# Kernel optimization log

Measured on AMD Instinct MI355X. Metric: run time of the kernel, lower is better.

The kernel has to match this reference:

```python
import jax, jax.numpy as jnp
import numpy as np

B, S, D_IN, H, G, HD = 1, 2048, 2048, 32, 8, 128
GS = H // G  # group_size = 4
D_OUT = H * HD  # 4096
EPS = 1e-6


def _rmsnorm(x, scale):
    # qwen3-compatible: compute in fp32 over last dim
    xf = x.astype(jnp.float32)
    var = jnp.mean(xf * xf, axis=-1, keepdims=True)
    return (xf * jax.lax.rsqrt(var + EPS) * scale).astype(x.dtype)


def _apply_rope(x, cos, sin):
    # x: [b, h, s, d]; cos/sin: [s, d]
    d2 = x.shape[-1] // 2
    x1, x2 = x[..., :d2], x[..., d2:]
    rotated = jnp.concatenate([-x2, x1], axis=-1)
    return (x * cos[None, None] + rotated * sin[None, None]).astype(x.dtype)


def setup_inputs() -> dict:
    key = jax.random.key(0)
    ks = jax.random.split(key, 8)
    x = jax.random.normal(ks[0], (B, S, D_IN), jnp.float32)
    mask = jnp.triu(jnp.ones((S, S), bool), k=1)  # causal: True = masked
    # RoPE tables [S, HD]
    inv_freq = 1.0 / (10000.0 ** (jnp.arange(0, HD, 2, dtype=jnp.float32) / HD))
    ang = jnp.arange(S, dtype=jnp.float32)[:, None] * inv_freq[None, :]
    ang = jnp.concatenate([ang, ang], axis=-1)
    cos, sin = jnp.cos(ang), jnp.sin(ang)
    std = 0.02
    Wq = jax.random.normal(ks[1], (D_IN, D_OUT), jnp.float32) * std
    Wk = jax.random.normal(ks[2], (D_IN, G * HD), jnp.float32) * std
    Wv = jax.random.normal(ks[3], (D_IN, G * HD), jnp.float32) * std
    Wo = jax.random.normal(ks[4], (D_OUT, D_IN), jnp.float32) * std
    q_scale = jnp.ones((HD,), jnp.float32)
    k_scale = jnp.ones((HD,), jnp.float32)
    return {"x": x, "mask": mask, "cos": cos, "sin": sin,
            "Wq": Wq, "Wk": Wk, "Wv": Wv, "Wo": Wo,
            "q_scale": q_scale, "k_scale": k_scale}


def reference(x, mask, cos, sin, Wq, Wk, Wv, Wo, q_scale, k_scale):
    b, s, _ = x.shape
    q = (x @ Wq).reshape(b, s, H, HD).transpose(0, 2, 1, 3)   # [b,H,s,hd]
    k = (x @ Wk).reshape(b, s, G, HD).transpose(0, 2, 1, 3)   # [b,G,s,hd]
    v = (x @ Wv).reshape(b, s, G, HD).transpose(0, 2, 1, 3)   # [b,G,s,hd]
    q = _rmsnorm(q, q_scale)
    k = _rmsnorm(k, k_scale)
    q = _apply_rope(q, cos[:s], sin[:s])
    k = _apply_rope(k, cos[:s], sin[:s])
    next_k, next_v = k, v  # cache (num_kv_groups heads)
    # GQA via broadcasting instead of repeat_interleave (same math)
    qg = q.reshape(b, G, GS, s, HD)
    scores = jnp.einsum('bgrsd,bgtd->bgrst', qg, k)           # [b,G,gs,s,s]
    scores = jnp.where(mask[None, None, None], -jnp.inf, scores)
    attn = jax.nn.softmax(scores / np.sqrt(HD).astype(np.float32), axis=-1)
    ctx = jnp.einsum('bgrst,bgtd->bgrsd', attn, v)            # [b,G,gs,s,hd]
    ctx = ctx.reshape(b, H, s, HD).transpose(0, 2, 1, 3).reshape(b, s, D_OUT)
    out = ctx @ Wo
    return out, next_k, next_v
```

## Files before the change

kernel.cpp:

```cpp
#include <hip/hip_runtime.h>

typedef unsigned short ushort_t;
typedef short short8 __attribute__((ext_vector_type(8)));
typedef float floatx4 __attribute__((ext_vector_type(4)));

#define S_LEN 2048
#define DIN   2048
#define NH    32
#define NG    8
#define HDIM  128
#define DOUT  4096
#define DKV   1024
#define QLD   6144

__device__ __forceinline__ float b2f(ushort_t u) {
  union { float f; unsigned u; } t; t.u = ((unsigned)u) << 16; return t.f;
}
__device__ __forceinline__ ushort_t f2b(float f) {
  union { float f; unsigned u; } t; t.f = f;
  unsigned v = t.u;
  v += 0x7FFFu + ((v >> 16) & 1u);
  return (ushort_t)(v >> 16);
}

__device__ __forceinline__ void glds16(const ushort_t* g, ushort_t* l) {
  __builtin_amdgcn_global_load_lds((const __attribute__((address_space(1))) void*)g,
                                   (__attribute__((address_space(3))) void*)l, 16, 0, 0);
}

__global__ __launch_bounds__(256) void tcast(const float* __restrict__ W,
                                             ushort_t* __restrict__ Wt,
                                             int N, int ldt) {
  __shared__ float t[32][33];
  const int bx = blockIdx.x * 32;
  const int by = blockIdx.y * 32;
  const int tx = threadIdx.x & 31;
  const int ty = threadIdx.x >> 5;
#pragma unroll
  for (int i = 0; i < 32; i += 8)
    t[ty + i][tx] = W[(size_t)(by + ty + i) * N + bx + tx];
  __syncthreads();
#pragma unroll
  for (int i = 0; i < 32; i += 8)
    Wt[(size_t)(bx + ty + i) * ldt + by + tx] = f2b(t[tx][ty + i]);
}

__global__ __launch_bounds__(256) void castx(const float* __restrict__ x,
                                             ushort_t* __restrict__ xb) {
  const size_t i = ((size_t)blockIdx.x * 256 + threadIdx.x) * 4;
  float4 v = *(const float4*)&x[i];
  union { int2 p; ushort_t s[4]; } w;
  w.s[0] = f2b(v.x); w.s[1] = f2b(v.y); w.s[2] = f2b(v.z); w.s[3] = f2b(v.w);
  *(int2*)&xb[i] = w.p;
}

template <int CF32, int BM>
__global__ __launch_bounds__(256) void gemm_glds(const ushort_t* __restrict__ A, int lda,
                                                 const ushort_t* __restrict__ Bt, int ldb,
                                                 void* __restrict__ Cp, int ldc, int K) {
  constexpr int MI = BM / 32;
  __shared__ __align__(16) ushort_t As[BM * 32];
  __shared__ __align__(16) ushort_t Bs[4096];
  const int tid  = threadIdx.x;
  const int m0   = blockIdx.y * BM;
  const int n0   = blockIdx.x * 128;
  const int wave = tid >> 6, lane = tid & 63;
  const int lrow = lane & 15, quad = lane >> 4;
  const int wm = (wave >> 1) * (BM / 2), wn = (wave & 1) * 64;

  floatx4 acc[MI][4];
#pragma unroll
  for (int mi = 0; mi < MI; mi++)
#pragma unroll
    for (int ni = 0; ni < 4; ni++)
#pragma unroll
      for (int j = 0; j < 4; j++) acc[mi][ni][j] = 0.0f;

  const ushort_t* ag0 = A + (size_t)(m0 + (tid >> 2)) * lda + (tid & 3) * 8;
  const ushort_t* ag1 = ag0 + (size_t)64 * lda;
  const ushort_t* bg0 = Bt + (size_t)(n0 + (tid >> 2)) * ldb + (tid & 3) * 8;
  const ushort_t* bg1 = bg0 + (size_t)64 * ldb;
  ushort_t* lA0 = As + wave * 512;
  ushort_t* lA1 = As + 2048 + wave * 512;
  ushort_t* lB0 = Bs + wave * 512;
  ushort_t* lB1 = Bs + 2048 + wave * 512;

  for (int k0 = 0; k0 < K; k0 += 32) {
    __syncthreads();
    glds16(ag0 + k0, lA0);
    if (BM == 128) glds16(ag1 + k0, lA1);
    glds16(bg0 + k0, lB0);
    glds16(bg1 + k0, lB1);
    __syncthreads();

    short8 af[MI], bf[4];
#pragma unroll
    for (int mi = 0; mi < MI; mi++)
      af[mi] = *(const short8*)&As[(wm + mi * 16 + lrow) * 32 + quad * 8];
#pragma unroll
    for (int ni = 0; ni < 4; ni++)
      bf[ni] = *(const short8*)&Bs[(wn + ni * 16 + lrow) * 32 + quad * 8];
#pragma unroll
    for (int mi = 0; mi < MI; mi++)
#pragma unroll
      for (int ni = 0; ni < 4; ni++)
        acc[mi][ni] = __builtin_amdgcn_mfma_f32_16x16x32_bf16(af[mi], bf[ni], acc[mi][ni], 0, 0, 0);
  }

#pragma unroll
  for (int mi = 0; mi < MI; mi++)
#pragma unroll
    for (int ni = 0; ni < 4; ni++)
#pragma unroll
      for (int i = 0; i < 4; i++) {
        const int row = m0 + wm + mi * 16 + quad * 4 + i;
        const int col = n0 + wn + ni * 16 + lrow;
        if (CF32) ((float*)Cp)[(size_t)row * ldc + col] = acc[mi][ni][i];
        else      ((ushort_t*)Cp)[(size_t)row * ldc + col] = f2b(acc[mi][ni][i]);
      }
}

__global__ __launch_bounds__(256) void norm_qk(ushort_t* __restrict__ qkv,
                                               const float* __restrict__ cosb,
                                               const float* __restrict__ sinb,
                                               const float* __restrict__ qs,
                                               const float* __restrict__ ks,
                                               ushort_t* __restrict__ kb) {
  const int idx  = blockIdx.x * 4 + (threadIdx.x >> 6);
  const int lane = threadIdx.x & 63;
  const int SH = S_LEN * NH;
  const float QSC = 0.08838834764831845f * 1.4426950408889634f;

  if (idx < SH) {
    const int s = idx >> 5, h = idx & 31;
    ushort_t* row = qkv + (size_t)s * QLD + h * HDIM;
    float x1 = b2f(row[lane]), x2 = b2f(row[lane + 64]);
    float ss = x1 * x1 + x2 * x2;
#pragma unroll
    for (int off = 1; off < 64; off <<= 1) ss += __shfl_xor(ss, off);
    const float inv = rsqrtf(ss * (1.0f / 128.0f) + 1e-6f);
    const float y1 = x1 * inv * qs[lane] * QSC;
    const float y2 = x2 * inv * qs[lane + 64] * QSC;
    const float c1 = cosb[s * HDIM + lane],      s1 = sinb[s * HDIM + lane];
    const float c2 = cosb[s * HDIM + lane + 64], s2 = sinb[s * HDIM + lane + 64];
    row[lane]      = f2b(y1 * c1 - y2 * s1);
    row[lane + 64] = f2b(y2 * c2 + y1 * s2);
  } else {
    const int j = idx - SH;
    const int s = j >> 3, g = j & 7;
    const ushort_t* row = qkv + (size_t)s * QLD + DOUT + g * HDIM;
    float x1 = b2f(row[lane]), x2 = b2f(row[lane + 64]);
    float ss = x1 * x1 + x2 * x2;
#pragma unroll
    for (int off = 1; off < 64; off <<= 1) ss += __shfl_xor(ss, off);
    const float inv = rsqrtf(ss * (1.0f / 128.0f) + 1e-6f);
    const float y1 = x1 * inv * ks[lane];
    const float y2 = x2 * inv * ks[lane + 64];
    const float c1 = cosb[s * HDIM + lane],      s1 = sinb[s * HDIM + lane];
    const float c2 = cosb[s * HDIM + lane + 64], s2 = sinb[s * HDIM + lane + 64];
    ushort_t* o = kb + ((size_t)g * S_LEN + s) * HDIM;
    o[lane]      = f2b(y1 * c1 - y2 * s1);
    o[lane + 64] = f2b(y2 * c2 + y1 * s2);
  }
}

__global__ __launch_bounds__(256) void vtrans(const ushort_t* __restrict__ qkv,
                                              ushort_t* __restrict__ vt) {
  __shared__ ushort_t t[64][65];
  const int g = blockIdx.x;
  const int s0 = blockIdx.y * 64, d0 = blockIdx.z * 64;
  const int tx = threadIdx.x & 63, ty = threadIdx.x >> 6;
#pragma unroll
  for (int i = 0; i < 64; i += 4)
    t[ty + i][tx] = qkv[(size_t)(s0 + ty + i) * QLD + DOUT + DKV + g * HDIM + d0 + tx];
  __syncthreads();
#pragma unroll
  for (int i = 0; i < 64; i += 4)
    vt[((size_t)(g * HDIM + d0 + ty + i)) * S_LEN + s0 + tx] = t[tx][ty + i];
}

__global__ __launch_bounds__(256, 2) void attn(ushort_t* QC,
                                               const ushort_t* __restrict__ Kb,
                                               const ushort_t* __restrict__ Vt) {
  __shared__ __align__(16) ushort_t Ks[8192];
  __shared__ __align__(16) ushort_t Vs[8192];
  __shared__ __align__(16) ushort_t Ps[64 * 72];
  const int h  = blockIdx.x;
  const int qt = 31 - blockIdx.y;
  const int g  = h >> 2;
  const int tid = threadIdx.x;
  const int wave = tid >> 6, lane = tid & 63;
  const int lrow = lane & 15, quad = lane >> 4;
  const ushort_t* Kg = Kb + (size_t)g * S_LEN * HDIM;
  const ushort_t* Vg = Vt + (size_t)g * HDIM * S_LEN;
  const int r0 = qt * 64;
  const int qrow0 = r0 + wave * 16;

  short8 qf[4];
#pragma unroll
  for (int kd = 0; kd < 4; kd++)
    qf[kd] = *(const short8*)&QC[(size_t)(qrow0 + lrow) * QLD + h * HDIM + kd * 32 + quad * 8];

  short8 vones;
#pragma unroll
  for (int j = 0; j < 8; j++) vones[j] = (lrow == 0) ? (short)0x3F80 : (short)0;

  floatx4 ctx[8], ctxl;
#pragma unroll
  for (int nd = 0; nd < 8; nd++)
#pragma unroll
    for (int j = 0; j < 4; j++) ctx[nd][j] = 0.0f;
#pragma unroll
  for (int j = 0; j < 4; j++) ctxl[j] = 0.0f;

  const ushort_t* kgl = Kg + (size_t)(wave * 16 + (lane >> 2)) * HDIM + (lane & 3) * 8;
  const ushort_t* vgl = Vg + (size_t)(wave * 32 + (lane >> 2)) * S_LEN + (lane & 3) * 8;

  for (int t0 = 0; t0 <= r0; t0 += 64) {
    __syncthreads();
#pragma unroll
    for (int i = 0; i < 4; i++)
      glds16(kgl + (size_t)t0 * HDIM + i * 32, Ks + i * 2048 + wave * 512);
#pragma unroll
    for (int i = 0; i < 4; i++)
      glds16(vgl + (size_t)((i >> 1) * 16) * S_LEN + t0 + (i & 1) * 32,
             Vs + (i & 1) * 4096 + (wave * 32 + (i >> 1) * 16) * 32);
    __syncthreads();

    floatx4 sacc[4];
#pragma unroll
    for (int ni = 0; ni < 4; ni++)
#pragma unroll
      for (int j = 0; j < 4; j++) sacc[ni][j] = 0.0f;
#pragma unroll
    for (int kd = 0; kd < 4; kd++) {
      short8 kf[4];
#pragma unroll
      for (int ni = 0; ni < 4; ni++)
        kf[ni] = *(const short8*)&Ks[kd * 2048 + (ni * 16 + lrow) * 32 + quad * 8];
#pragma unroll
      for (int ni = 0; ni < 4; ni++)
        sacc[ni] = __builtin_amdgcn_mfma_f32_16x16x32_bf16(qf[kd], kf[ni], sacc[ni], 0, 0, 0);
    }

    const bool diag = (t0 == r0);
#pragma unroll
    for (int ni = 0; ni < 4; ni++)
#pragma unroll
      for (int i = 0; i < 4; i++) {
        float sv = sacc[ni][i];
        if (diag && (t0 + ni * 16 + lrow > qrow0 + quad * 4 + i)) sv = -1e30f;
        sacc[ni][i] = exp2f(sv - 17.0f);
      }

#pragma unroll
    for (int ni = 0; ni < 4; ni++)
#pragma unroll
      for (int i = 0; i < 4; i++)
        Ps[(wave * 16 + quad * 4 + i) * 72 + ni * 16 + lrow] = f2b(sacc[ni][i]);
    asm volatile("s_waitcnt lgkmcnt(0)" ::: "memory");

#pragma unroll
    for (int kt = 0; kt < 2; kt++) {
      const short8 pf = *(const short8*)&Ps[(wave * 16 + lrow) * 72 + kt * 32 + quad * 8];
      ctxl = __builtin_amdgcn_mfma_f32_16x16x32_bf16(pf, vones, ctxl, 0, 0, 0);
#pragma unroll
      for (int nd = 0; nd < 8; nd++) {
        const short8 vf = *(const short8*)&Vs[kt * 4096 + (nd * 16 + lrow) * 32 + quad * 8];
        ctx[nd] = __builtin_amdgcn_mfma_f32_16x16x32_bf16(pf, vf, ctx[nd], 0, 0, 0);
      }
    }
  }

  float invl[4];
#pragma unroll
  for (int i = 0; i < 4; i++) invl[i] = 1.0f / __shfl(ctxl[i], lane & 48);

  __syncthreads();
  ushort_t* Es = (wave < 2) ? Ks : Vs;
  const int eb = (wave & 1) * 16;
#pragma unroll
  for (int i = 0; i < 4; i++)
#pragma unroll
    for (int nd = 0; nd < 8; nd++)
      Es[(eb + quad * 4 + i) * 136 + nd * 16 + lrow] = f2b(ctx[nd][i] * invl[i]);
  asm volatile("s_waitcnt lgkmcnt(0)" ::: "memory");
  const int erow = lane >> 4;
  const int ecol = (lane & 15) * 8;
#pragma unroll
  for (int rr = 0; rr < 4; rr++) {
    int4 v = *(const int4*)&Es[(eb + rr * 4 + erow) * 136 + ecol];
    *(int4*)&QC[(size_t)(r0 + wave * 16 + rr * 4 + erow) * QLD + h * HDIM + ecol] = v;
  }
}

__global__ __launch_bounds__(256) void fink(const ushort_t* __restrict__ kb,
                                            float* __restrict__ nk) {
  const size_t e = ((size_t)blockIdx.x * 256 + threadIdx.x) * 8;
  union { int4 v; ushort_t s[8]; } u;
  u.v = *(const int4*)&kb[e];
#pragma unroll
  for (int j = 0; j < 8; j++) nk[e + j] = b2f(u.s[j]);
}

__global__ __launch_bounds__(256) void finv(const ushort_t* __restrict__ qkv,
                                            float* __restrict__ nv) {
  const int s = blockIdx.x;
  const int g = threadIdx.x >> 5, d4 = (threadIdx.x & 31) * 4;
  union { short4 v; ushort_t s[4]; } u;
  u.v = *(const short4*)&qkv[(size_t)s * QLD + DOUT + DKV + g * HDIM + d4];
  float4 o;
  o.x = b2f(u.s[0]); o.y = b2f(u.s[1]); o.z = b2f(u.s[2]); o.w = b2f(u.s[3]);
  *(float4*)&nv[((size_t)g * S_LEN + s) * HDIM + d4] = o;
}

extern "C" void kernel_launch(void* const* d_in, const int* in_sizes, int n_in,
                              void* d_out, int out_size, void* d_ws, size_t ws_size,
                              hipStream_t stream) {
  const float* x    = (const float*)d_in[0];
  const float* cosb = (const float*)d_in[2];
  const float* sinb = (const float*)d_in[3];
  const float* Wq   = (const float*)d_in[4];
  const float* Wk   = (const float*)d_in[5];
  const float* Wv   = (const float*)d_in[6];
  const float* Wo   = (const float*)d_in[7];
  const float* qs   = (const float*)d_in[8];
  const float* ks   = (const float*)d_in[9];

  float* outf = (float*)d_out;
  float* nkf  = outf + (size_t)S_LEN * DIN;
  float* nvf  = nkf + (size_t)NG * S_LEN * HDIM;

  const size_t MiB = 1024 * 1024;
  ushort_t* WallT = (ushort_t*)d_out;
  ushort_t* xb    = (ushort_t*)((char*)d_out + 24 * MiB);
  ushort_t* WoT   = (ushort_t*)((char*)d_out + 16 * MiB);
  ushort_t* vt    = (ushort_t*)d_out;
  ushort_t* qkv   = (ushort_t*)d_ws;
  ushort_t* kb    = (ushort_t*)((char*)d_ws + 24 * MiB);

  tcast<<<dim3(128, 64), 256, 0, stream>>>(Wq, WallT, DOUT, DIN);
  tcast<<<dim3(32, 64), 256, 0, stream>>>(Wk, WallT + (size_t)4096 * DIN, DKV, DIN);
  tcast<<<dim3(32, 64), 256, 0, stream>>>(Wv, WallT + (size_t)5120 * DIN, DKV, DIN);
  castx<<<4096, 256, 0, stream>>>(x, xb);

  gemm_glds<0, 128><<<dim3(48, 16), 256, 0, stream>>>(xb, DIN, WallT, DIN, qkv, QLD, DIN);

  tcast<<<dim3(64, 128), 256, 0, stream>>>(Wo, WoT, DIN, DOUT);

  norm_qk<<<(S_LEN * NH + S_LEN * NG) / 4, 256, 0, stream>>>(qkv, cosb, sinb, qs, ks, kb);

  vtrans<<<dim3(NG, S_LEN / 64, HDIM / 64), 256, 0, stream>>>(qkv, vt);

  attn<<<dim3(NH, 32), 256, 0, stream>>>(qkv, kb, vt);

  gemm_glds<1, 64><<<dim3(16, 32), 256, 0, stream>>>(qkv, QLD, WoT, DOUT, outf, DIN, DOUT);

  fink<<<1024, 256, 0, stream>>>(kb, nkf);
  finv<<<S_LEN, 256, 0, stream>>>(qkv, nvf);
}
```

Baseline: 399.8 us.

## Double-buffer LDS tiles with XOR swizzle in GEMM and attention

Both the projection GEMM and the attention kernel now use two LDS buffers. The next K-tile (or K/V tile) is loaded directly into LDS while the current one is computed, which replaces the two-barrier load-then-compute loop with one barrier per step. The 16-byte column chunks are also XOR-swizzled on both the write and read side to cut LDS bank conflicts. The cost is double the shared memory: attention goes from about 41 KB to about 74 KB per block, which may reduce occupancy under launch_bounds(256,2). The GEMM loop also assumes K/32 is even, which holds for the K values used here.

```diff
diff --git a/kernel.cpp b/kernel.cpp
--- a/kernel.cpp
+++ b/kernel.cpp
@@ -59,8 +59,8 @@
                                                  const ushort_t* __restrict__ Bt, int ldb,
                                                  void* __restrict__ Cp, int ldc, int K) {
   constexpr int MI = BM / 32;
-  __shared__ __align__(16) ushort_t As[BM * 32];
-  __shared__ __align__(16) ushort_t Bs[4096];
+  __shared__ __align__(16) ushort_t As[2][BM * 32];
+  __shared__ __align__(16) ushort_t Bs[2][4096];
   const int tid  = threadIdx.x;
   const int m0   = blockIdx.y * BM;
   const int n0   = blockIdx.x * 128;
@@ -76,35 +76,51 @@
 #pragma unroll
       for (int j = 0; j < 4; j++) acc[mi][ni][j] = 0.0f;
 
-  const ushort_t* ag0 = A + (size_t)(m0 + (tid >> 2)) * lda + (tid & 3) * 8;
+  const int sc = ((tid & 3) ^ ((tid >> 3) & 3)) * 8;
+  const ushort_t* ag0 = A + (size_t)(m0 + (tid >> 2)) * lda + sc;
   const ushort_t* ag1 = ag0 + (size_t)64 * lda;
-  const ushort_t* bg0 = Bt + (size_t)(n0 + (tid >> 2)) * ldb + (tid & 3) * 8;
+  const ushort_t* bg0 = Bt + (size_t)(n0 + (tid >> 2)) * ldb + sc;
   const ushort_t* bg1 = bg0 + (size_t)64 * ldb;
-  ushort_t* lA0 = As + wave * 512;
-  ushort_t* lA1 = As + 2048 + wave * 512;
-  ushort_t* lB0 = Bs + wave * 512;
-  ushort_t* lB1 = Bs + 2048 + wave * 512;
-
-  for (int k0 = 0; k0 < K; k0 += 32) {
-    __syncthreads();
-    glds16(ag0 + k0, lA0);
-    if (BM == 128) glds16(ag1 + k0, lA1);
-    glds16(bg0 + k0, lB0);
-    glds16(bg1 + k0, lB1);
-    __syncthreads();
-
-    short8 af[MI], bf[4];
+  const int so = wave * 512;
+
+  auto stage = [&](int k0, int b) {
+    glds16(ag0 + k0, &As[b][so]);
+    if constexpr (BM == 128) glds16(ag1 + k0, &As[b][2048 + so]);
+    glds16(bg0 + k0, &Bs[b][so]);
+    glds16(bg1 + k0, &Bs[b][2048 + so]);
+  };
+
+  const int rq = (quad ^ ((lrow >> 1) & 3)) * 8;
+
+  auto compute = [&](int b) {
+    short8 af[MI], bfr[4];
 #pragma unroll
     for (int mi = 0; mi < MI; mi++)
-      af[mi] = *(const short8*)&As[(wm + mi * 16 + lrow) * 32 + quad * 8];
-#pragma unroll
-    for (int ni = 0; ni < 4; ni++)
-      bf[ni] = *(const short8*)&Bs[(wn + ni * 16 + lrow) * 32 + quad * 8];
+      af[mi] = *(const short8*)&As[b][(wm + mi * 16 + lrow) * 32 + rq];
+#pragma unroll
+    for (int ni = 0; ni < 4; ni++)
+      bfr[ni] = *(const short8*)&Bs[b][(wn + ni * 16 + lrow) * 32 + rq];
 #pragma unroll
     for (int mi = 0; mi < MI; mi++)
 #pragma unroll
       for (int ni = 0; ni < 4; ni++)
-        acc[mi][ni] = __builtin_amdgcn_mfma_f32_16x16x32_bf16(af[mi], bf[ni], acc[mi][ni], 0, 0, 0);
+        acc[mi][ni] = __builtin_amdgcn_mfma_f32_16x16x32_bf16(af[mi], bfr[ni], acc[mi][ni], 0, 0, 0);
+  };
+
+  stage(0, 0);
+  asm volatile("s_waitcnt vmcnt(0)" ::: "memory");
+  __builtin_amdgcn_s_barrier();
+
+  const int NT = K >> 5;
+  for (int t = 0; t < NT; t += 2) {
+    stage((t + 1) << 5, 1);
+    compute(0);
+    asm volatile("s_waitcnt vmcnt(0)" ::: "memory");
+    __builtin_amdgcn_s_barrier();
+    if (t + 2 < NT) stage((t + 2) << 5, 0);
+    compute(1);
+    asm volatile("s_waitcnt vmcnt(0)" ::: "memory");
+    __builtin_amdgcn_s_barrier();
   }
 
 #pragma unroll
@@ -182,8 +198,8 @@
 __global__ __launch_bounds__(256, 2) void attn(ushort_t* QC,
                                                const ushort_t* __restrict__ Kb,
                                                const ushort_t* __restrict__ Vt) {
-  __shared__ __align__(16) ushort_t Ks[8192];
-  __shared__ __align__(16) ushort_t Vs[8192];
+  __shared__ __align__(16) ushort_t Ks[2][8192];
+  __shared__ __align__(16) ushort_t Vs[2][8192];
   __shared__ __align__(16) ushort_t Ps[64 * 72];
   const int h  = blockIdx.x;
   const int qt = 31 - blockIdx.y;
@@ -213,19 +229,31 @@
 #pragma unroll
   for (int j = 0; j < 4; j++) ctxl[j] = 0.0f;
 
-  const ushort_t* kgl = Kg + (size_t)(wave * 16 + (lane >> 2)) * HDIM + (lane & 3) * 8;
-  const ushort_t* vgl = Vg + (size_t)(wave * 32 + (lane >> 2)) * S_LEN + (lane & 3) * 8;
-
-  for (int t0 = 0; t0 <= r0; t0 += 64) {
-    __syncthreads();
+  const int swz = ((lane & 3) ^ ((lane >> 3) & 3)) * 8;
+  const ushort_t* kgl = Kg + (size_t)(wave * 16 + (lane >> 2)) * HDIM + swz;
+  const ushort_t* vgl = Vg + (size_t)(wave * 32 + (lane >> 2)) * S_LEN + swz;
+
+  auto stageKV = [&](int t0, int b) {
 #pragma unroll
     for (int i = 0; i < 4; i++)
-      glds16(kgl + (size_t)t0 * HDIM + i * 32, Ks + i * 2048 + wave * 512);
+      glds16(kgl + (size_t)t0 * HDIM + i * 32, &Ks[b][i * 2048 + wave * 512]);
 #pragma unroll
     for (int i = 0; i < 4; i++)
       glds16(vgl + (size_t)((i >> 1) * 16) * S_LEN + t0 + (i & 1) * 32,
-             Vs + (i & 1) * 4096 + (wave * 32 + (i >> 1) * 16) * 32);
-    __syncthreads();
+             &Vs[b][(i & 1) * 4096 + (wave * 32 + (i >> 1) * 16) * 32]);
+  };
+
+  const int rq = (quad ^ ((lrow >> 1) & 3)) * 8;
+
+  stageKV(0, 0);
+  asm volatile("s_waitcnt vmcnt(0)" ::: "memory");
+  __builtin_amdgcn_s_barrier();
+
+  int buf = 0;
+  for (int t0 = 0; t0 <= r0; t0 += 64) {
+    if (t0 + 64 <= r0) stageKV(t0 + 64, buf ^ 1);
+    const ushort_t* Kc = Ks[buf];
+    const ushort_t* Vc = Vs[buf];
 
     floatx4 sacc[4];
 #pragma unroll
@@ -237,7 +265,7 @@
       short8 kf[4];
 #pragma unroll
       for (int ni = 0; ni < 4; ni++)
-        kf[ni] = *(const short8*)&Ks[kd * 2048 + (ni * 16 + lrow) * 32 + quad * 8];
+        kf[ni] = *(const short8*)&Kc[kd * 2048 + (ni * 16 + lrow) * 32 + rq];
 #pragma unroll
       for (int ni = 0; ni < 4; ni++)
         sacc[ni] = __builtin_amdgcn_mfma_f32_16x16x32_bf16(qf[kd], kf[ni], sacc[ni], 0, 0, 0);
@@ -266,10 +294,14 @@
       ctxl = __builtin_amdgcn_mfma_f32_16x16x32_bf16(pf, vones, ctxl, 0, 0, 0);
 #pragma unroll
       for (int nd = 0; nd < 8; nd++) {
-        const short8 vf = *(const short8*)&Vs[kt * 4096 + (nd * 16 + lrow) * 32 + quad * 8];
+        const short8 vf = *(const short8*)&Vc[kt * 4096 + (nd * 16 + lrow) * 32 + rq];
         ctx[nd] = __builtin_amdgcn_mfma_f32_16x16x32_bf16(pf, vf, ctx[nd], 0, 0, 0);
       }
     }
+
+    asm volatile("s_waitcnt vmcnt(0)" ::: "memory");
+    __builtin_amdgcn_s_barrier();
+    buf ^= 1;
   }
 
   float invl[4];
@@ -277,7 +309,7 @@
   for (int i = 0; i < 4; i++) invl[i] = 1.0f / __shfl(ctxl[i], lane & 48);
 
   __syncthreads();
-  ushort_t* Es = (wave < 2) ? Ks : Vs;
+  ushort_t* Es = (wave < 2) ? Ks[0] : Vs[0];
   const int eb = (wave & 1) * 16;
 #pragma unroll
   for (int i = 0; i < 4; i++)
```

Result: slower. 410.6 us (+2.7%).
